# Optimization experiments

Hardware: AMD Instinct MI355X
Metric: run time of the kernel (lower is better)

The kernel has to match this reference:

```python
import jax, jax.numpy as jnp
import numpy as np

NBIT = 4          # weight bit-width
GROUP_SIZE = 128  # weight quantization group size (divides k)
HAS_WEIGHT_ZEROS = True


def _quant_dequant_weights(w, group_size=GROUP_SIZE, nbit=NBIT, has_zeros=HAS_WEIGHT_ZEROS):
    # Mirrors torchao _quantize + quantize_per_channel_group, then dequantizes
    # (the native kernel dequantizes inline with the matmul; math is identical).
    qmin = -(1 << (nbit - 1))
    qmax = (1 << (nbit - 1)) - 1
    n, k = w.shape
    g = w.reshape(-1, group_size)                      # [n*k/gs, gs]
    vmin = g.min(axis=1, keepdims=True)
    vmax = g.max(axis=1, keepdims=True)
    scales = (vmax - vmin) / (qmax - qmin)             # per-group scale
    if has_zeros:
        zeros = qmin - jnp.round(vmin / scales)
    else:
        zeros = jnp.zeros_like(scales)
    q = jnp.clip(jnp.round(g / scales) + zeros, qmin, qmax)
    deq = (q - zeros) * scales
    return deq.reshape(n, k)


def _dyn_quant_dequant_act(x):
    # Dynamic per-token (per-row) asymmetric int8 activation quantization.
    qmin, qmax = -128, 127
    xmin = x.min(axis=-1, keepdims=True)
    xmax = x.max(axis=-1, keepdims=True)
    scale = (xmax - xmin) / (qmax - qmin)
    zero = qmin - jnp.round(xmin / scale)
    q = jnp.clip(jnp.round(x / scale) + zero, qmin, qmax)
    return (q - zero) * scale


def setup_inputs() -> dict:
    key = jax.random.key(0)
    k1, k2 = jax.random.split(key)
    x = jax.random.normal(k1, (4, 2048, 4096), dtype=jnp.float32)
    weights = jax.random.normal(k2, (4096, 4096), dtype=jnp.float32) * 0.02
    return {"x": x, "weights": weights}


def reference(x, weights):
    w_deq = _quant_dequant_weights(weights)            # [n, k]
    x_deq = _dyn_quant_dequant_act(x)                  # [..., m, k]
    # y[..., m, n] = x_deq @ w_deq^T
    return jnp.einsum('bmk,nk->bmn', x_deq, w_deq)
```

## Files before the change

### kernel.cpp

```cpp
#include <hip/hip_runtime.h>
#include <hip/hip_bf16.h>
#include <cfloat>

typedef __attribute__((ext_vector_type(8))) short bf16x8;
typedef __attribute__((ext_vector_type(4))) float f32x4;

#define M_DIM 8192
#define N_DIM 4096
#define K_DIM 4096

__device__ inline ushort f2bf(float f) {
    unsigned u = __float_as_uint(f);
    unsigned r = (u + 0x7FFFu + ((u >> 16) & 1u)) >> 16;
    return (ushort)r;
}

#define SWZ(x) ((x) ^ ((((x) >> 7) & 7) << 4))

__global__ __launch_bounds__(256) void w_dequant(const float* __restrict__ w,
                                                 ushort* __restrict__ wq) {
    int g = blockIdx.x * 4 + (threadIdx.x >> 6);
    int lane = threadIdx.x & 63;
    const float* src = w + (size_t)g * 128;
    float2 v = *(const float2*)(src + lane * 2);
    float mn = fminf(v.x, v.y), mx = fmaxf(v.x, v.y);
#pragma unroll
    for (int s = 1; s < 64; s <<= 1) {
        mn = fminf(mn, __shfl_xor(mn, s));
        mx = fmaxf(mx, __shfl_xor(mx, s));
    }
    float scale = (mx - mn) / 15.0f;
    float zero  = -8.0f - rintf(mn / scale);
    float q0 = fminf(fmaxf(rintf(v.x / scale) + zero, -8.0f), 7.0f);
    float q1 = fminf(fmaxf(rintf(v.y / scale) + zero, -8.0f), 7.0f);
    ushort2 o;
    o.x = f2bf((q0 - zero) * scale);
    o.y = f2bf((q1 - zero) * scale);
    *(ushort2*)(wq + (size_t)g * 128 + lane * 2) = o;
}

__global__ __launch_bounds__(256) void act_qdq(const float* __restrict__ x,
                                               ushort* __restrict__ xq) {
    __shared__ float smn[4], smx[4];
    int row = blockIdx.x;
    const float* xr = x + (size_t)row * K_DIM;
    ushort* xo = xq + (size_t)row * K_DIM;
    int t = threadIdx.x;
    float4 v[4];
    float mn = FLT_MAX, mx = -FLT_MAX;
#pragma unroll
    for (int i = 0; i < 4; i++) {
        v[i] = ((const float4*)xr)[t + i * 256];
        mn = fminf(mn, fminf(fminf(v[i].x, v[i].y), fminf(v[i].z, v[i].w)));
        mx = fmaxf(mx, fmaxf(fmaxf(v[i].x, v[i].y), fmaxf(v[i].z, v[i].w)));
    }
#pragma unroll
    for (int s = 1; s < 64; s <<= 1) {
        mn = fminf(mn, __shfl_xor(mn, s));
        mx = fmaxf(mx, __shfl_xor(mx, s));
    }
    int w = t >> 6;
    if ((t & 63) == 0) { smn[w] = mn; smx[w] = mx; }
    __syncthreads();
    mn = fminf(fminf(smn[0], smn[1]), fminf(smn[2], smn[3]));
    mx = fmaxf(fmaxf(smx[0], smx[1]), fmaxf(smx[2], smx[3]));
    float scale = (mx - mn) / 255.0f;
    float zero  = -128.0f - rintf(mn / scale);
#pragma unroll
    for (int i = 0; i < 4; i++) {
        ushort4 o;
        float q;
        q = fminf(fmaxf(rintf(v[i].x / scale) + zero, -128.0f), 127.0f); o.x = f2bf((q - zero) * scale);
        q = fminf(fmaxf(rintf(v[i].y / scale) + zero, -128.0f), 127.0f); o.y = f2bf((q - zero) * scale);
        q = fminf(fmaxf(rintf(v[i].z / scale) + zero, -128.0f), 127.0f); o.z = f2bf((q - zero) * scale);
        q = fminf(fmaxf(rintf(v[i].w / scale) + zero, -128.0f), 127.0f); o.w = f2bf((q - zero) * scale);
        ((ushort4*)xo)[t + i * 256] = o;
    }
}

#define BM 256
#define BN 256
#define BK 64
#define NT (K_DIM / BK)

__global__ __launch_bounds__(512, 1) void gemm_bt8(const ushort* __restrict__ A,
                                                   const ushort* __restrict__ B,
                                                   float* __restrict__ C) {
    __shared__ __align__(16) ushort As[2][BM * BK];
    __shared__ __align__(16) ushort Bs[2][BN * BK];

    const int nbx = N_DIM / BN;
    const int nwg = (M_DIM / BM) * nbx;
    int bid = blockIdx.x;
    bid = (bid & 7) * (nwg / 8) + (bid >> 3);
    int mb = bid / nbx, nb = bid % nbx;
    size_t m0 = (size_t)mb * BM, n0 = (size_t)nb * BN;

    const int t = threadIdx.x;
    const int w = t >> 6, lane = t & 63;
    const int wm = w >> 2, wn = w & 3;
    const int lr = lane & 15;
    const int lk = (lane >> 4) << 3;

    const ushort* Ab = A + m0 * K_DIM;
    const ushort* Bb = B + n0 * K_DIM;

    const int mask7 = (lr & 7) << 4;
    const int lp0 = lr * 128 + ((lk * 2) ^ mask7);
    const int lp1 = lr * 128 + ((64 + lk * 2) ^ mask7);
    const char* A_k0 = (const char*)As + wm * 4096 + lp0;
    const char* A_k1 = (const char*)As + wm * 4096 + lp1;
    const char* B_k0 = (const char*)Bs + wn * 8192 + lp0;
    const char* B_k1 = (const char*)Bs + wn * 8192 + lp1;

    int off_q[4], dst_q[4];
#pragma unroll
    for (int rq = 0; rq < 4; rq++) {
        int base = rq * 8192 + w * 1024;
        int lg = SWZ(base + lane * 16);
        off_q[rq] = (lg >> 7) * K_DIM + ((lg & 127) >> 1);
        dst_q[rq] = base;
    }

    auto STAGE = [&](int T, int qq) {
        if (T >= NT) return;
        int d = T & 1;
        bool isA = qq < 4;
        int rq = qq & 3;
        ushort* l = isA ? As[d] : Bs[d];
        const ushort* g = (isA ? Ab : Bb) + (size_t)T * BK + off_q[rq];
        __builtin_amdgcn_global_load_lds(
            (const __attribute__((address_space(1))) unsigned int*)g,
            (__attribute__((address_space(3))) unsigned int*)((char*)l + dst_q[rq]),
            16, 0, 0);
    };

    f32x4 acc[8][4] = {};
    bf16x8 afr[2][2];
    bf16x8 bfr[4][2];

#define LOADA(d, q) do {                                                          \
    _Pragma("unroll") for (int ii = 0; ii < 2; ii++) {                            \
        afr[ii][0] = *(const bf16x8*)(A_k0 + (d) * 32768 + ((q) * 64 + ii * 16) * 128); \
        afr[ii][1] = *(const bf16x8*)(A_k1 + (d) * 32768 + ((q) * 64 + ii * 16) * 128); \
    } } while (0)
#define LOADB(d) do {                                                             \
    _Pragma("unroll") for (int ni = 0; ni < 4; ni++) {                            \
        bfr[ni][0] = *(const bf16x8*)(B_k0 + (d) * 32768 + ni * 2048);            \
        bfr[ni][1] = *(const bf16x8*)(B_k1 + (d) * 32768 + ni * 2048);            \
    } } while (0)

#define PHASE(d, q, sT1, sq1, sT2, sq2, vm) do {                                  \
    if ((q) == 0) LOADB(d);                                                       \
    LOADA(d, q);                                                                  \
    STAGE(sT1, sq1);                                                              \
    STAGE(sT2, sq2);                                                              \
    __builtin_amdgcn_s_barrier();                                                 \
    asm volatile("s_waitcnt lgkmcnt(0)" ::: "memory");                            \
    __builtin_amdgcn_sched_barrier(0);                                            \
    __builtin_amdgcn_s_setprio(1);                                                \
    _Pragma("unroll") for (int kk = 0; kk < 2; kk++)                              \
    _Pragma("unroll") for (int ii = 0; ii < 2; ii++)                              \
    _Pragma("unroll") for (int ni = 0; ni < 4; ni++)                              \
        acc[(q) * 2 + ii][ni] = __builtin_amdgcn_mfma_f32_16x16x32_bf16(          \
            afr[ii][kk], bfr[ni][kk], acc[(q) * 2 + ii][ni], 0, 0, 0);            \
    __builtin_amdgcn_s_setprio(0);                                                \
    if ((vm) == 1) asm volatile("s_waitcnt vmcnt(6)" ::: "memory");               \
    if ((vm) == 2) asm volatile("s_waitcnt vmcnt(0)" ::: "memory");               \
    __builtin_amdgcn_s_barrier();                                                 \
  } while (0)

    STAGE(0, 0); STAGE(0, 1); STAGE(0, 2); STAGE(0, 3);
    STAGE(0, 4); STAGE(0, 5); STAGE(0, 6); STAGE(0, 7);
    STAGE(1, 4); STAGE(1, 5); STAGE(1, 6); STAGE(1, 7);
    STAGE(1, 0); STAGE(1, 1);
    asm volatile("s_waitcnt vmcnt(6)" ::: "memory");
    __builtin_amdgcn_s_barrier();

#pragma unroll 1
    for (int i = 0; i < NT / 2 - 1; i++) {
        int T0 = 2 * i;
        PHASE(0, 0, T0 + 1, 2, T0 + 1, 3, 0);
        PHASE(0, 1, T0 + 2, 4, T0 + 2, 5, 0);
        PHASE(0, 2, T0 + 2, 6, T0 + 2, 7, 0);
        PHASE(0, 3, T0 + 2, 0, T0 + 2, 1, 1);
        PHASE(1, 0, T0 + 2, 2, T0 + 2, 3, 0);
        PHASE(1, 1, T0 + 3, 4, T0 + 3, 5, 0);
        PHASE(1, 2, T0 + 3, 6, T0 + 3, 7, 0);
        PHASE(1, 3, T0 + 3, 0, T0 + 3, 1, 1);
    }

    PHASE(0, 0, NT - 1, 2, NT - 1, 3, 0);
    PHASE(0, 1, NT, 0, NT, 0, 0);
    PHASE(0, 2, NT, 0, NT, 0, 0);
    PHASE(0, 3, NT, 0, NT, 0, 2);
    PHASE(1, 0, NT, 0, NT, 0, 0);
    PHASE(1, 1, NT, 0, NT, 0, 0);
    PHASE(1, 2, NT, 0, NT, 0, 0);
    PHASE(1, 3, NT, 0, NT, 0, 0);
#undef PHASE
#undef LOADA
#undef LOADB

    int fq = lane >> 4;
#pragma unroll
    for (int mi = 0; mi < 8; mi++) {
#pragma unroll
        for (int ni = 0; ni < 4; ni++) {
#pragma unroll
            for (int r = 0; r < 4; r++) {
                size_t crow = m0 + (mi >> 1) * 64 + wm * 32 + (mi & 1) * 16 + fq * 4 + r;
                C[crow * N_DIM + n0 + wn * 64 + ni * 16 + lr] = acc[mi][ni][r];
            }
        }
    }
}

extern "C" void kernel_launch(void* const* d_in, const int* in_sizes, int n_in,
                              void* d_out, int out_size, void* d_ws, size_t ws_size,
                              hipStream_t stream) {
    const float* x = (const float*)d_in[0];
    const float* w = (const float*)d_in[1];
    float* out = (float*)d_out;

    ushort* wq = (ushort*)d_ws;
    ushort* xq = (ushort*)((char*)d_ws + (size_t)N_DIM * K_DIM * 2);

    hipLaunchKernelGGL(w_dequant, dim3((N_DIM * K_DIM / 128) / 4), dim3(256), 0, stream, w, wq);
    hipLaunchKernelGGL(act_qdq, dim3(M_DIM), dim3(256), 0, stream, x, xq);
    hipLaunchKernelGGL(gemm_bt8, dim3((M_DIM / BM) * (N_DIM / BN)), dim3(512), 0, stream, xq, wq, out);
}
```

Before: 307.1 us.

## Double-buffer LDS fragment registers to prefetch next phase during MFMA

Splits the A and B register fragments into two slots, so each phase reads the next phase's fragments from LDS while the MFMAs run on the current slot. One of the two barriers per phase is removed, the LDS wait moves after the MFMA block, and the vmcnt wait schedule is reworked, including a prologue preload. The aim is to hide LDS read latency behind matrix math and to cut synchronization. In exchange it needs more VGPRs, which can hurt occupancy, and the hand-tuned wait counts must still be correct.

After: 401.0 us. +30.6%, slower.

```diff
diff --git a/kernel.cpp b/kernel.cpp
--- a/kernel.cpp
+++ b/kernel.cpp
@@ -136,68 +136,72 @@
     };
 
     f32x4 acc[8][4] = {};
-    bf16x8 afr[2][2];
-    bf16x8 bfr[4][2];
-
-#define LOADA(d, q) do {                                                          \
+    bf16x8 afr[2][2][2];
+    bf16x8 bfr[2][4][2];
+
+#define LOADA(S, d, q) do {                                                       \
     _Pragma("unroll") for (int ii = 0; ii < 2; ii++) {                            \
-        afr[ii][0] = *(const bf16x8*)(A_k0 + (d) * 32768 + ((q) * 64 + ii * 16) * 128); \
-        afr[ii][1] = *(const bf16x8*)(A_k1 + (d) * 32768 + ((q) * 64 + ii * 16) * 128); \
+        afr[S][ii][0] = *(const bf16x8*)(A_k0 + (d) * 32768 + ((q) * 64 + ii * 16) * 128); \
+        afr[S][ii][1] = *(const bf16x8*)(A_k1 + (d) * 32768 + ((q) * 64 + ii * 16) * 128); \
     } } while (0)
-#define LOADB(d) do {                                                             \
+#define LOADB(db) do {                                                            \
     _Pragma("unroll") for (int ni = 0; ni < 4; ni++) {                            \
-        bfr[ni][0] = *(const bf16x8*)(B_k0 + (d) * 32768 + ni * 2048);            \
-        bfr[ni][1] = *(const bf16x8*)(B_k1 + (d) * 32768 + ni * 2048);            \
+        bfr[db][ni][0] = *(const bf16x8*)(B_k0 + (db) * 32768 + ni * 2048);       \
+        bfr[db][ni][1] = *(const bf16x8*)(B_k1 + (db) * 32768 + ni * 2048);       \
     } } while (0)
 
-#define PHASE(d, q, sT1, sq1, sT2, sq2, vm) do {                                  \
-    if ((q) == 0) LOADB(d);                                                       \
-    LOADA(d, q);                                                                  \
+#define PHASE(q, S, dc, qn, dn, sT1, sq1, sT2, sq2, vm) do {                      \
+    if ((qn) == 0) LOADB(dn);                                                     \
+    LOADA((S) ^ 1, dn, qn);                                                       \
     STAGE(sT1, sq1);                                                              \
     STAGE(sT2, sq2);                                                              \
-    __builtin_amdgcn_s_barrier();                                                 \
-    asm volatile("s_waitcnt lgkmcnt(0)" ::: "memory");                            \
     __builtin_amdgcn_sched_barrier(0);                                            \
     __builtin_amdgcn_s_setprio(1);                                                \
     _Pragma("unroll") for (int kk = 0; kk < 2; kk++)                              \
     _Pragma("unroll") for (int ii = 0; ii < 2; ii++)                              \
     _Pragma("unroll") for (int ni = 0; ni < 4; ni++)                              \
         acc[(q) * 2 + ii][ni] = __builtin_amdgcn_mfma_f32_16x16x32_bf16(          \
-            afr[ii][kk], bfr[ni][kk], acc[(q) * 2 + ii][ni], 0, 0, 0);            \
+            afr[S][ii][kk], bfr[dc][ni][kk], acc[(q) * 2 + ii][ni], 0, 0, 0);     \
     __builtin_amdgcn_s_setprio(0);                                                \
+    asm volatile("s_waitcnt lgkmcnt(0)" ::: "memory");                            \
     if ((vm) == 1) asm volatile("s_waitcnt vmcnt(6)" ::: "memory");               \
     if ((vm) == 2) asm volatile("s_waitcnt vmcnt(0)" ::: "memory");               \
     __builtin_amdgcn_s_barrier();                                                 \
+    __builtin_amdgcn_sched_barrier(0);                                            \
   } while (0)
 
     STAGE(0, 0); STAGE(0, 1); STAGE(0, 2); STAGE(0, 3);
     STAGE(0, 4); STAGE(0, 5); STAGE(0, 6); STAGE(0, 7);
     STAGE(1, 4); STAGE(1, 5); STAGE(1, 6); STAGE(1, 7);
     STAGE(1, 0); STAGE(1, 1);
-    asm volatile("s_waitcnt vmcnt(6)" ::: "memory");
+    asm volatile("s_waitcnt vmcnt(4)" ::: "memory");
     __builtin_amdgcn_s_barrier();
+    LOADB(0);
+    LOADA(0, 0, 0);
+    asm volatile("s_waitcnt lgkmcnt(0)" ::: "memory");
+    __builtin_amdgcn_sched_barrier(0);
 
 #pragma unroll 1
     for (int i = 0; i < NT / 2 - 1; i++) {
         int T0 = 2 * i;
-        PHASE(0, 0, T0 + 1, 2, T0 + 1, 3, 0);
-        PHASE(0, 1, T0 + 2, 4, T0 + 2, 5, 0);
-        PHASE(0, 2, T0 + 2, 6, T0 + 2, 7, 0);
-        PHASE(0, 3, T0 + 2, 0, T0 + 2, 1, 1);
-        PHASE(1, 0, T0 + 2, 2, T0 + 2, 3, 0);
-        PHASE(1, 1, T0 + 3, 4, T0 + 3, 5, 0);
-        PHASE(1, 2, T0 + 3, 6, T0 + 3, 7, 0);
-        PHASE(1, 3, T0 + 3, 0, T0 + 3, 1, 1);
-    }
-
-    PHASE(0, 0, NT - 1, 2, NT - 1, 3, 0);
-    PHASE(0, 1, NT, 0, NT, 0, 0);
-    PHASE(0, 2, NT, 0, NT, 0, 0);
-    PHASE(0, 3, NT, 0, NT, 0, 2);
-    PHASE(1, 0, NT, 0, NT, 0, 0);
-    PHASE(1, 1, NT, 0, NT, 0, 0);
-    PHASE(1, 2, NT, 0, NT, 0, 0);
-    PHASE(1, 3, NT, 0, NT, 0, 0);
+        PHASE(0, 0, 0, 1, 0, T0 + 1, 2, T0 + 1, 3, 1);
+        PHASE(1, 1, 0, 2, 0, T0 + 2, 4, T0 + 2, 5, 0);
+        PHASE(2, 0, 0, 3, 0, T0 + 2, 6, T0 + 2, 7, 1);
+        PHASE(3, 1, 0, 0, 1, T0 + 2, 0, T0 + 2, 1, 0);
+        PHASE(0, 0, 1, 1, 1, T0 + 2, 2, T0 + 2, 3, 1);
+        PHASE(1, 1, 1, 2, 1, T0 + 3, 4, T0 + 3, 5, 0);
+        PHASE(2, 0, 1, 3, 1, T0 + 3, 6, T0 + 3, 7, 1);
+        PHASE(3, 1, 1, 0, 0, T0 + 3, 0, T0 + 3, 1, 0);
+    }
+
+    PHASE(0, 0, 0, 1, 0, NT - 1, 2, NT - 1, 3, 1);
+    PHASE(1, 1, 0, 2, 0, NT, 0, NT, 0, 0);
+    PHASE(2, 0, 0, 3, 0, NT, 0, NT, 0, 2);
+    PHASE(3, 1, 0, 0, 1, NT, 0, NT, 0, 0);
+    PHASE(0, 0, 1, 1, 1, NT, 0, NT, 0, 0);
+    PHASE(1, 1, 1, 2, 1, NT, 0, NT, 0, 0);
+    PHASE(2, 0, 1, 3, 1, NT, 0, NT, 0, 0);
+    PHASE(3, 1, 1, 0, 0, NT, 0, NT, 0, 0);
 #undef PHASE
 #undef LOADA
 #undef LOADB
```

## Double-buffer A fragments and prefetch next phase's LDS reads during MFMA

Applied to the files above, without the earlier changes.

Register-double-buffers the A fragments so each phase loads the next phase's A data from LDS while running MFMAs on the current buffer. It drops the per-phase pre-MFMA barrier and lgkmcnt(0) wait, and changes the vmcnt schedule so waits happen every phase. The goal is to hide LDS read latency and cut synchronisation. In exchange it uses more VGPRs and loosens ordering. Without the lgkmcnt wait, correctness depends on the compiler inserting waits for register dependencies, and LDS reads may race with the global_load_lds staging writes.

Result: no change. 308.0 us (+0.3%).

```diff
diff --git a/kernel.cpp b/kernel.cpp
--- a/kernel.cpp
+++ b/kernel.cpp
@@ -136,34 +136,33 @@
     };
 
     f32x4 acc[8][4] = {};
-    bf16x8 afr[2][2];
+    bf16x8 afr[2][2][2];
     bf16x8 bfr[4][2];
 
-#define LOADA(d, q) do {                                                          \
-    _Pragma("unroll") for (int ii = 0; ii < 2; ii++) {                            \
-        afr[ii][0] = *(const bf16x8*)(A_k0 + (d) * 32768 + ((q) * 64 + ii * 16) * 128); \
-        afr[ii][1] = *(const bf16x8*)(A_k1 + (d) * 32768 + ((q) * 64 + ii * 16) * 128); \
-    } } while (0)
+#define LOADA(S, d, q) do {                                                       \
+    _Pragma("unroll") for (int ii = 0; ii < 2; ii++)                              \
+        afr[S][ii][0] = *(const bf16x8*)(A_k0 + (d) * 32768 + ((q) * 64 + ii * 16) * 128); \
+    _Pragma("unroll") for (int ii = 0; ii < 2; ii++)                              \
+        afr[S][ii][1] = *(const bf16x8*)(A_k1 + (d) * 32768 + ((q) * 64 + ii * 16) * 128); \
+    } while (0)
 #define LOADB(d) do {                                                             \
-    _Pragma("unroll") for (int ni = 0; ni < 4; ni++) {                            \
+    _Pragma("unroll") for (int ni = 0; ni < 4; ni++)                              \
         bfr[ni][0] = *(const bf16x8*)(B_k0 + (d) * 32768 + ni * 2048);            \
+    _Pragma("unroll") for (int ni = 0; ni < 4; ni++)                              \
         bfr[ni][1] = *(const bf16x8*)(B_k1 + (d) * 32768 + ni * 2048);            \
-    } } while (0)
-
-#define PHASE(d, q, sT1, sq1, sT2, sq2, vm) do {                                  \
+    } while (0)
+
+#define PHASE(d, q, S, dn, qn, sT1, sq1, sT2, sq2, vm) do {                       \
     if ((q) == 0) LOADB(d);                                                       \
-    LOADA(d, q);                                                                  \
+    LOADA((S) ^ 1, dn, qn);                                                       \
     STAGE(sT1, sq1);                                                              \
     STAGE(sT2, sq2);                                                              \
-    __builtin_amdgcn_s_barrier();                                                 \
-    asm volatile("s_waitcnt lgkmcnt(0)" ::: "memory");                            \
-    __builtin_amdgcn_sched_barrier(0);                                            \
     __builtin_amdgcn_s_setprio(1);                                                \
     _Pragma("unroll") for (int kk = 0; kk < 2; kk++)                              \
     _Pragma("unroll") for (int ii = 0; ii < 2; ii++)                              \
     _Pragma("unroll") for (int ni = 0; ni < 4; ni++)                              \
         acc[(q) * 2 + ii][ni] = __builtin_amdgcn_mfma_f32_16x16x32_bf16(          \
-            afr[ii][kk], bfr[ni][kk], acc[(q) * 2 + ii][ni], 0, 0, 0);            \
+            afr[S][ii][kk], bfr[ni][kk], acc[(q) * 2 + ii][ni], 0, 0, 0);         \
     __builtin_amdgcn_s_setprio(0);                                                \
     if ((vm) == 1) asm volatile("s_waitcnt vmcnt(6)" ::: "memory");               \
     if ((vm) == 2) asm volatile("s_waitcnt vmcnt(0)" ::: "memory");               \
@@ -176,28 +175,29 @@
     STAGE(1, 0); STAGE(1, 1);
     asm volatile("s_waitcnt vmcnt(6)" ::: "memory");
     __builtin_amdgcn_s_barrier();
+    LOADA(0, 0, 0);
 
 #pragma unroll 1
     for (int i = 0; i < NT / 2 - 1; i++) {
         int T0 = 2 * i;
-        PHASE(0, 0, T0 + 1, 2, T0 + 1, 3, 0);
-        PHASE(0, 1, T0 + 2, 4, T0 + 2, 5, 0);
-        PHASE(0, 2, T0 + 2, 6, T0 + 2, 7, 0);
-        PHASE(0, 3, T0 + 2, 0, T0 + 2, 1, 1);
-        PHASE(1, 0, T0 + 2, 2, T0 + 2, 3, 0);
-        PHASE(1, 1, T0 + 3, 4, T0 + 3, 5, 0);
-        PHASE(1, 2, T0 + 3, 6, T0 + 3, 7, 0);
-        PHASE(1, 3, T0 + 3, 0, T0 + 3, 1, 1);
-    }
-
-    PHASE(0, 0, NT - 1, 2, NT - 1, 3, 0);
-    PHASE(0, 1, NT, 0, NT, 0, 0);
-    PHASE(0, 2, NT, 0, NT, 0, 0);
-    PHASE(0, 3, NT, 0, NT, 0, 2);
-    PHASE(1, 0, NT, 0, NT, 0, 0);
-    PHASE(1, 1, NT, 0, NT, 0, 0);
-    PHASE(1, 2, NT, 0, NT, 0, 0);
-    PHASE(1, 3, NT, 0, NT, 0, 0);
+        PHASE(0, 0, 0, 0, 1, T0 + 1, 2, T0 + 1, 3, 1);
+        PHASE(0, 1, 1, 0, 2, T0 + 2, 4, T0 + 2, 5, 1);
+        PHASE(0, 2, 0, 0, 3, T0 + 2, 6, T0 + 2, 7, 1);
+        PHASE(0, 3, 1, 1, 0, T0 + 2, 0, T0 + 2, 1, 1);
+        PHASE(1, 0, 0, 1, 1, T0 + 2, 2, T0 + 2, 3, 1);
+        PHASE(1, 1, 1, 1, 2, T0 + 3, 4, T0 + 3, 5, 1);
+        PHASE(1, 2, 0, 1, 3, T0 + 3, 6, T0 + 3, 7, 1);
+        PHASE(1, 3, 1, 0, 0, T0 + 3, 0, T0 + 3, 1, 1);
+    }
+
+    PHASE(0, 0, 0, 0, 1, NT - 1, 2, NT - 1, 3, 1);
+    PHASE(0, 1, 1, 0, 2, NT, 0, NT, 0, 2);
+    PHASE(0, 2, 0, 0, 3, NT, 0, NT, 0, 0);
+    PHASE(0, 3, 1, 1, 0, NT, 0, NT, 0, 0);
+    PHASE(1, 0, 0, 1, 1, NT, 0, NT, 0, 0);
+    PHASE(1, 1, 1, 1, 2, NT, 0, NT, 0, 0);
+    PHASE(1, 2, 0, 1, 3, NT, 0, NT, 0, 0);
+    PHASE(1, 3, 1, 0, 0, NT, 0, NT, 0, 0);
 #undef PHASE
 #undef LOADA
 #undef LOADB
```
